# Performance work log

Hardware: AMD Instinct MI355X
Metric: run time of the kernel (lower is better)

The kernel has to match this reference:

```python
import jax, jax.numpy as jnp
import numpy as np

B, N, M, D = 4, 512, 512, 128
H, DOUT = 256, 128

def setup_inputs() -> dict:
    key = jax.random.key(0)
    k = jax.random.split(key, 4)
    X = jax.random.normal(k[0], (B, N, D), dtype=jnp.float32)
    Y = jax.random.normal(k[1], (B, M, D), dtype=jnp.float32)
    W1 = jax.random.normal(k[2], (2 * D, H), dtype=jnp.float32) / np.sqrt(2 * D)
    b1 = jnp.zeros((H,), dtype=jnp.float32)
    W2 = jax.random.normal(k[3], (H, DOUT), dtype=jnp.float32) / np.sqrt(H)
    b2 = jnp.zeros((DOUT,), dtype=jnp.float32)
    return {"X": X, "Y": Y, "W1": W1, "b1": b1, "W2": W2, "b2": b2}

def reference(X, Y, W1, b1, W2, b2):
    # pairs[b,n,m,:] = concat(Y[b,m], X[b,n])  -> [B,N,M,2D]
    n_ = X.shape[1]
    m_ = Y.shape[1]
    Ye = jnp.broadcast_to(Y[:, None, :, :], (X.shape[0], n_, m_, Y.shape[-1]))
    Xe = jnp.broadcast_to(X[:, :, None, :], (X.shape[0], n_, m_, X.shape[-1]))
    pairs = jnp.concatenate([Ye, Xe], axis=-1)
    # pointwise MLP: Linear -> ReLU -> Linear
    hdn = jax.nn.relu(jnp.einsum('bnmd,dh->bnmh', pairs, W1) + b1)
    Z = jnp.einsum('bnmh,ho->bnmo', hdn, W2) + b2
    # pool='sum' over the M (neighbor) dimension
    return jnp.sum(Z, axis=2)  # [B, N, DOUT]
```

## Files before the change

### kernel.cpp

```cpp
#include <hip/hip_runtime.h>

#define BB    4
#define NN    512
#define MM    512
#define DD    128
#define HH    256
#define DOUTC 128

typedef float v2f __attribute__((ext_vector_type(2)));
typedef float v4f __attribute__((ext_vector_type(4)));

__global__ __launch_bounds__(1024) void precompute_ac(
    const float* __restrict__ X, const float* __restrict__ Y,
    const float* __restrict__ W1, const float* __restrict__ b1,
    float* __restrict__ AC, float* __restrict__ SAT)
{
    __shared__ __align__(16) float rows[16][DD];
    __shared__ __align__(16) v4f mrg[3][4][4][64];
    const int bid = blockIdx.x;
    const int t   = threadIdx.x;

    if (bid < 256) {
        const int isC = bid >> 7;
        const int r0  = (bid & 127) * 16;
        const float* src = isC ? X : Y;

        if (t < 512)
            reinterpret_cast<v4f*>(&rows[0][0])[t] =
                reinterpret_cast<const v4f*>(src + (size_t)r0 * DD)[t];
        __syncthreads();

        const int hq = t & 63;
        const int dq = (t >> 6) & 3;
        const int rs = t >> 8;
        const int d0 = dq * 32;
        const float* wp = W1 + (isC ? DD * HH : 0) + hq * 4;

        v4f acc[4];
#pragma unroll
        for (int r = 0; r < 4; ++r) acc[r] = (v4f){0.f, 0.f, 0.f, 0.f};

#pragma unroll 2
        for (int dg = 0; dg < 32; dg += 4) {
            const int d = d0 + dg;
            const v4f w0 = *reinterpret_cast<const v4f*>(&wp[(d + 0) * HH]);
            const v4f w1 = *reinterpret_cast<const v4f*>(&wp[(d + 1) * HH]);
            const v4f w2 = *reinterpret_cast<const v4f*>(&wp[(d + 2) * HH]);
            const v4f w3 = *reinterpret_cast<const v4f*>(&wp[(d + 3) * HH]);
#pragma unroll
            for (int r = 0; r < 4; ++r) {
                const v4f rv = *reinterpret_cast<const v4f*>(&rows[rs * 4 + r][d]);
                acc[r] += w0 * rv.x;
                acc[r] += w1 * rv.y;
                acc[r] += w2 * rv.z;
                acc[r] += w3 * rv.w;
            }
        }

        if (dq > 0) {
#pragma unroll
            for (int r = 0; r < 4; ++r) mrg[dq - 1][rs][r][hq] = acc[r];
        }
        __syncthreads();
        if (dq == 0) {
#pragma unroll
            for (int r = 0; r < 4; ++r) {
#pragma unroll
                for (int p = 0; p < 3; ++p) acc[r] += mrg[p][rs][r][hq];
            }
            v4f bias = (v4f){0.f, 0.f, 0.f, 0.f};
            if (isC) bias = *reinterpret_cast<const v4f*>(&b1[hq * 4]);
#pragma unroll
            for (int r = 0; r < 4; ++r)
                *reinterpret_cast<v4f*>(
                    &AC[((size_t)(isC * 2048 + r0 + rs * 4 + r)) * HH + hq * 4]) =
                    acc[r] + bias;
        }
    } else {
        const int half = t >> 9;
        const int bb   = (bid - 256) * 2 + half;
        const int tt   = t & 511;
        float* scr = &rows[0][0];

        const int d  = tt & 127;
        const int mq = tt >> 7;
        const float* yp = Y + ((size_t)(bb * MM + mq * 128)) * DD + d;
        float s = 0.f;
#pragma unroll 4
        for (int i = 0; i < 128; ++i) s += yp[(size_t)i * DD];
        scr[half * 512 + mq * 128 + d] = s;
        __syncthreads();

        if (tt < 256) {
            const float* base = scr + half * 512;
            float sat = 0.f;
#pragma unroll 4
            for (int dd = 0; dd < 128; ++dd) {
                const float ys = base[dd] + base[128 + dd] +
                                 base[256 + dd] + base[384 + dd];
                sat = fmaf(ys, W1[dd * HH + tt], sat);
            }
            SAT[bb * HH + tt] = sat;
        }
    }
}

__global__ __launch_bounds__(256) void abs_main(
    const float* __restrict__ A, const float* __restrict__ C,
    float* __restrict__ part)
{
    __shared__ __align__(16) v4f mergeA[3][8][64];
    const int bid = blockIdx.x;
    const int mc  = bid & 3;
    const int nt  = (bid >> 2) & 63;
    const int b   = bid >> 8;
    const int t   = threadIdx.x;
    const int l   = t & 63;
    const int w   = t >> 6;
    const int h0  = l * 4;
    const int n0  = nt * 8;

    const float* Cb = C + ((size_t)(b * NN + n0)) * HH + h0;
    v2f c01[8], c23[8];
#pragma unroll
    for (int j = 0; j < 8; ++j) {
        const v4f cv = *reinterpret_cast<const v4f*>(&Cb[(size_t)j * HH]);
        c01[j] = (v2f){cv.x, cv.y};
        c23[j] = (v2f){cv.z, cv.w};
    }

    float acc[8][4];
#pragma unroll
    for (int j = 0; j < 8; ++j)
#pragma unroll
        for (int u = 0; u < 4; ++u) acc[j][u] = 0.f;

    const float* Ab = A + ((size_t)(b * MM + mc * 128 + w * 32)) * HH + h0;
#pragma unroll 4
    for (int i = 0; i < 32; ++i) {
        const v4f a = *reinterpret_cast<const v4f*>(&Ab[(size_t)i * HH]);
        const v2f a01 = (v2f){a.x, a.y};
        const v2f a23 = (v2f){a.z, a.w};
#pragma unroll
        for (int j = 0; j < 8; ++j) {
            const v2f s01 = a01 + c01[j];
            const v2f s23 = a23 + c23[j];
            acc[j][0] += fabsf(s01.x);
            acc[j][1] += fabsf(s01.y);
            acc[j][2] += fabsf(s23.x);
            acc[j][3] += fabsf(s23.y);
        }
    }

    if (w > 0) {
#pragma unroll
        for (int j = 0; j < 8; ++j)
            mergeA[w - 1][j][l] = (v4f){acc[j][0], acc[j][1], acc[j][2], acc[j][3]};
    }
    __syncthreads();
    if (w == 0) {
#pragma unroll
        for (int j = 0; j < 8; ++j) {
            v4f s = (v4f){acc[j][0], acc[j][1], acc[j][2], acc[j][3]};
#pragma unroll
            for (int p = 0; p < 3; ++p) s += mergeA[p][j][l];
            *reinterpret_cast<v4f*>(&part[((size_t)bid * 8 + j) * HH + h0]) = s;
        }
    }
}

__global__ __launch_bounds__(512) void epilogue(
    const float* __restrict__ part, const float* __restrict__ SAT,
    const float* __restrict__ C, const float* __restrict__ W2,
    const float* __restrict__ b2, float* __restrict__ out)
{
    __shared__ __align__(16) float Sl[4][HH];
    __shared__ __align__(16) v4f red[3 * 128];
    const int bn0 = blockIdx.x * 4;
    const int b   = bn0 >> 9;
    const int t   = threadIdx.x;

    if (t < 256) {
        const int h    = t;
        const float sv = SAT[b * HH + h];
        const int nt   = (bn0 & 511) >> 3;
#pragma unroll
        for (int r = 0; r < 4; ++r) {
            const int bn = bn0 + r;
            const int j  = bn & 7;
            float ab = 0.f;
#pragma unroll
            for (int mcq = 0; mcq < 4; ++mcq)
                ab += part[((size_t)((b * 256 + nt * 4 + mcq)) * 8 + j) * HH + h];
            const float cv = C[(size_t)bn * HH + h];
            Sl[r][h] = 0.5f * (sv + 512.f * cv + ab);
        }
    }
    __syncthreads();

    const int o0 = (t & 31) * 4;
    const int r  = (t >> 5) & 3;
    const int kq = t >> 7;
    const int k0 = kq * 64;
    v4f a4 = (v4f){0.f, 0.f, 0.f, 0.f};
    const float* w2p = W2 + o0;
#pragma unroll 4
    for (int k = k0; k < k0 + 64; k += 4) {
        const v4f sv = *reinterpret_cast<const v4f*>(&Sl[r][k]);
        const v4f wA = *reinterpret_cast<const v4f*>(&w2p[(k + 0) * DOUTC]);
        const v4f wB = *reinterpret_cast<const v4f*>(&w2p[(k + 1) * DOUTC]);
        const v4f wC = *reinterpret_cast<const v4f*>(&w2p[(k + 2) * DOUTC]);
        const v4f wD = *reinterpret_cast<const v4f*>(&w2p[(k + 3) * DOUTC]);
        a4 += wA * sv.x;
        a4 += wB * sv.y;
        a4 += wC * sv.z;
        a4 += wD * sv.w;
    }
    if (kq) red[(kq - 1) * 128 + (t & 127)] = a4;
    __syncthreads();
    if (kq == 0) {
#pragma unroll
        for (int p = 0; p < 3; ++p) a4 += red[p * 128 + (t & 127)];
        a4 += 512.f * (*reinterpret_cast<const v4f*>(&b2[o0]));
        *reinterpret_cast<v4f*>(&out[(size_t)(bn0 + r) * DOUTC + o0]) = a4;
    }
}

extern "C" void kernel_launch(void* const* d_in, const int* in_sizes, int n_in,
                              void* d_out, int out_size, void* d_ws, size_t ws_size,
                              hipStream_t stream) {
    const float* X  = (const float*)d_in[0];
    const float* Y  = (const float*)d_in[1];
    const float* W1 = (const float*)d_in[2];
    const float* b1 = (const float*)d_in[3];
    const float* W2 = (const float*)d_in[4];
    const float* b2 = (const float*)d_in[5];
    float* out = (float*)d_out;

    float* AC   = (float*)d_ws;
    float* A    = AC;
    float* Cm   = AC + 2048 * HH;
    float* part = AC + 4096 * HH;
    float* SAT  = part + (size_t)1024 * 8 * HH;

    hipLaunchKernelGGL(precompute_ac, dim3(258), dim3(1024), 0, stream,
                       X, Y, W1, b1, AC, SAT);
    hipLaunchKernelGGL(abs_main, dim3(1024), dim3(256), 0, stream,
                       A, Cm, part);
    hipLaunchKernelGGL(epilogue, dim3(512), dim3(512), 0, stream,
                       part, SAT, Cm, W2, b2, out);
}
```

Baseline: 52.82 us.

## Double-buffer A rows through LDS with rotated start chunk in abs_main

The abs_main inner loop now stages A rows through a double-buffered LDS tile. Each iteration prefetches the next 16-row chunk into registers while computing on the current chunk, so global load latency overlaps with the abs-sum arithmetic. The chunk order is rotated per block so that concurrent blocks touch different A rows first, spreading cache/channel traffic. The cost is extra LDS traffic, a barrier every chunk, and 32KB of LDS per block, which may reduce occupancy.

```diff
diff --git a/kernel.cpp b/kernel.cpp
--- a/kernel.cpp
+++ b/kernel.cpp
@@ -109,7 +109,7 @@
     const float* __restrict__ A, const float* __restrict__ C,
     float* __restrict__ part)
 {
-    __shared__ __align__(16) v4f mergeA[3][8][64];
+    __shared__ __align__(16) v4f lds[2048];
     const int bid = blockIdx.x;
     const int mc  = bid & 3;
     const int nt  = (bid >> 2) & 63;
@@ -119,6 +119,7 @@
     const int w   = t >> 6;
     const int h0  = l * 4;
     const int n0  = nt * 8;
+    const int rot = (nt * 3 + mc) & 7;
 
     const float* Cb = C + ((size_t)(b * NN + n0)) * HH + h0;
     v2f c01[8], c23[8];
@@ -135,27 +136,60 @@
 #pragma unroll
         for (int u = 0; u < 4; ++u) acc[j][u] = 0.f;
 
-    const float* Ab = A + ((size_t)(b * MM + mc * 128 + w * 32)) * HH + h0;
-#pragma unroll 4
-    for (int i = 0; i < 32; ++i) {
-        const v4f a = *reinterpret_cast<const v4f*>(&Ab[(size_t)i * HH]);
-        const v2f a01 = (v2f){a.x, a.y};
-        const v2f a23 = (v2f){a.z, a.w};
-#pragma unroll
-        for (int j = 0; j < 8; ++j) {
-            const v2f s01 = a01 + c01[j];
-            const v2f s23 = a23 + c23[j];
-            acc[j][0] += fabsf(s01.x);
-            acc[j][1] += fabsf(s01.y);
-            acc[j][2] += fabsf(s23.x);
-            acc[j][3] += fabsf(s23.y);
-        }
-    }
-
+    const float* Ab = A + ((size_t)(b * MM + mc * 128)) * HH;
+
+    v4f st[4];
+#pragma unroll
+    for (int k = 0; k < 4; ++k)
+        st[k] = *reinterpret_cast<const v4f*>(
+            Ab + (size_t)(rot * 16 + k * 4 + w) * HH + l * 4);
+#pragma unroll
+    for (int k = 0; k < 4; ++k)
+        lds[(k * 4 + w) * 64 + l] = st[k];
+    __syncthreads();
+
+    int cur = 0;
+    for (int s = 0; s < 8; ++s) {
+        if (s < 7) {
+            const int sp = (s + 1 + rot) & 7;
+#pragma unroll
+            for (int k = 0; k < 4; ++k)
+                st[k] = *reinterpret_cast<const v4f*>(
+                    Ab + (size_t)(sp * 16 + k * 4 + w) * HH + l * 4);
+        }
+
+#pragma unroll
+        for (int i = 0; i < 4; ++i) {
+            const v4f a = lds[cur * 1024 + (w * 4 + i) * 64 + l];
+            const v2f a01 = (v2f){a.x, a.y};
+            const v2f a23 = (v2f){a.z, a.w};
+#pragma unroll
+            for (int j = 0; j < 8; ++j) {
+                const v2f s01 = a01 + c01[j];
+                const v2f s23 = a23 + c23[j];
+                acc[j][0] += fabsf(s01.x);
+                acc[j][1] += fabsf(s01.y);
+                acc[j][2] += fabsf(s23.x);
+                acc[j][3] += fabsf(s23.y);
+            }
+        }
+
+        if (s < 7) {
+            const int nxt = cur ^ 1;
+#pragma unroll
+            for (int k = 0; k < 4; ++k)
+                lds[nxt * 1024 + (k * 4 + w) * 64 + l] = st[k];
+            __syncthreads();
+            cur = nxt;
+        }
+    }
+
+    __syncthreads();
     if (w > 0) {
 #pragma unroll
         for (int j = 0; j < 8; ++j)
-            mergeA[w - 1][j][l] = (v4f){acc[j][0], acc[j][1], acc[j][2], acc[j][3]};
+            lds[(w - 1) * 512 + j * 64 + l] =
+                (v4f){acc[j][0], acc[j][1], acc[j][2], acc[j][3]};
     }
     __syncthreads();
     if (w == 0) {
@@ -163,7 +197,7 @@
         for (int j = 0; j < 8; ++j) {
             v4f s = (v4f){acc[j][0], acc[j][1], acc[j][2], acc[j][3]};
 #pragma unroll
-            for (int p = 0; p < 3; ++p) s += mergeA[p][j][l];
+            for (int p = 0; p < 3; ++p) s += lds[p * 512 + j * 64 + l];
             *reinterpret_cast<v4f*>(&part[((size_t)bid * 8 + j) * HH + h0]) = s;
         }
     }
```

After: 55.82 us. 1.06x slower.
